# Kernel tuning notes

Measured on AMD Instinct MI355X. Metric: run time of the kernel, lower is better.

## Reference

```python
import jax, jax.numpy as jnp
import numpy as np

KERNEL_DIMS = 16
BOND = 4
OUT = 10
STEP = KERNEL_DIMS // 4          # 4
D = STEP * STEP                  # in_dims = 16
BATCH = 128


def setup_inputs() -> dict:
    key = jax.random.key(0)
    ks = jax.random.split(key, 9)
    d, b = D, BOND
    inp = {
        "inputs": jax.random.normal(ks[0], (BATCH, KERNEL_DIMS, KERNEL_DIMS, 1), dtype=jnp.float32),
        # entanglers (stddev 1e-4 as in the original init)
        "e1": jax.random.normal(ks[1], (d, d, d, d, b, b, b, b), dtype=jnp.float32) * 1e-4,
        "e2": jax.random.normal(ks[2], (b, b, b, b, b, b, b, b), dtype=jnp.float32) * 1e-4,
        # isometries (stddev 1e-5), leg orders exactly as in the source
        "iso1_0": jax.random.normal(ks[3], (d, d, d, b, b), dtype=jnp.float32) * 1e-5,
        "iso1_1": jax.random.normal(ks[4], (d, d, b, d, b), dtype=jnp.float32) * 1e-5,
        "iso1_2": jax.random.normal(ks[5], (d, b, d, d, b), dtype=jnp.float32) * 1e-5,
        "iso1_3": jax.random.normal(ks[6], (b, d, d, d, b), dtype=jnp.float32) * 1e-5,
        "iso2": jax.random.normal(ks[7], (b, b, b, b, OUT), dtype=jnp.float32) * 1e-5,
        "bias": jnp.zeros((OUT,), dtype=jnp.float32),
    }
    return inp


def reference(inputs, e1, e2, iso1_0, iso1_1, iso1_2, iso1_3, iso2, bias):
    B = inputs.shape[0]
    # 4x4 grid of step x step patches, each flattened to D features.
    # patch index k = i*4 + ii, matching the python loops in the original.
    xv = (inputs[..., 0]
          .reshape(B, 4, STEP, 4, STEP)
          .transpose(0, 1, 3, 2, 4)
          .reshape(B, 16, D))           # [B, 16, D]
    p = lambda k: xv[:, k, :]

    # entangler 1: legs 0-3 contract with patches 5,6,9,10; legs 4-7 go to isometries.
    v = jnp.einsum('abcdefgh,Ba,Bb,Bc,Bd->Befgh', e1, p(5), p(6), p(9), p(10))  # [B,b,b,b,b]

    # layer-1 isometries: contract their three patch legs, keep (bond-in m, bond-out o).
    t0 = jnp.einsum('ijkmo,Bi,Bj,Bk->Bmo', iso1_0, p(0), p(1), p(4))    # m = e1 leg4
    t1 = jnp.einsum('ijmko,Bi,Bj,Bk->Bmo', iso1_1, p(2), p(3), p(7))    # m = e1 leg5
    t2 = jnp.einsum('imjko,Bi,Bj,Bk->Bmo', iso1_2, p(8), p(12), p(13))  # m = e1 leg6
    t3 = jnp.einsum('mijko,Bi,Bj,Bk->Bmo', iso1_3, p(11), p(14), p(15)) # m = e1 leg7

    # fuse entangler-1 output with the four isometry bond maps -> entangler-2 inputs.
    w = jnp.einsum('Befgh,Bea,Bfb,Bgc,Bhd->Babcd', v, t0, t1, t2, t3)   # [B,b,b,b,b]

    # entangler 2 then top isometry into output_dims.
    out = jnp.einsum('Babcd,abcdefgh,efghC->BC', w, e2, iso2)           # [B, OUT]
    return out + bias
```

## Files before the change

### kernel.cpp

```cpp
#include <hip/hip_runtime.h>


#define KC 64

typedef __attribute__((ext_vector_type(8))) short bf16x8;
typedef __attribute__((ext_vector_type(4))) float f32x4;

__device__ __forceinline__ void splitf(float x, short& h, short& l) {
    unsigned u = __builtin_bit_cast(unsigned, x);
    h = (short)(u >> 16);
    float hf = __builtin_bit_cast(float, u & 0xFFFF0000u);
    float rem = x - hf;
    l = (short)(__builtin_bit_cast(unsigned, rem) >> 16);
}

__global__ void k1_xv(const float* __restrict__ in, float* __restrict__ xv) {
    int b = blockIdx.x, t = threadIdx.x;
    int k = t >> 4, d = t & 15;
    int row = (k >> 2) * 4 + (d >> 2);
    int col = (k & 3) * 4 + (d & 3);
    xv[b * 256 + t] = in[b * 256 + row * 16 + col];
}

__global__ void __launch_bounds__(256) k2_iso(
        const float* __restrict__ i0, const float* __restrict__ i1,
        const float* __restrict__ i2, const float* __restrict__ i3,
        const float* __restrict__ xv, float* __restrict__ tt) {
    int b = blockIdx.x, iso = blockIdx.y;
    int t = threadIdx.x;

    const int pid0[4] = {0, 2, 8, 11};
    const int pid1[4] = {1, 3, 12, 14};
    const int pid2[4] = {4, 7, 13, 15};
    const int siA[4] = {4096, 4096, 4096, 1024};
    const int sjA[4] = {256, 256, 64, 64};
    const int skA[4] = {16, 4, 4, 4};
    const int smA[4] = {4, 64, 1024, 16384};

    const float* iso_p = (iso == 0) ? i0 : (iso == 1) ? i1 : (iso == 2) ? i2 : i3;

    __shared__ float pX[16], pY[16], pZ[16];
    if (t < 16)      pX[t]      = xv[b * 256 + pid0[iso] * 16 + t];
    else if (t < 32) pY[t - 16] = xv[b * 256 + pid1[iso] * 16 + (t - 16)];
    else if (t < 48) pZ[t - 32] = xv[b * 256 + pid2[iso] * 16 + (t - 32)];
    __syncthreads();

    int i = t >> 4, j = t & 15;
    float pxy = pX[i] * pY[j];
    int sk = skA[iso], sm = smA[iso];
    const float* basep = iso_p + i * siA[iso] + j * sjA[iso];

    float acc[16];
#pragma unroll
    for (int mo = 0; mo < 16; ++mo) acc[mo] = 0.f;

    for (int k = 0; k < 16; ++k) {
        float w = pxy * pZ[k];
        const float* kp = basep + k * sk;
#pragma unroll
        for (int m = 0; m < 4; ++m) {
            float4 v = *(const float4*)(kp + m * sm);
            acc[m * 4 + 0] += w * v.x;
            acc[m * 4 + 1] += w * v.y;
            acc[m * 4 + 2] += w * v.z;
            acc[m * 4 + 3] += w * v.w;
        }
    }

    __shared__ float red[16 * 257];
    __shared__ float part[256];
#pragma unroll
    for (int mo = 0; mo < 16; ++mo) red[mo * 257 + t] = acc[mo];
    __syncthreads();
    int mo = t & 15, seg = t >> 4;
    float s = 0.f;
#pragma unroll
    for (int u = 0; u < 16; ++u) s += red[mo * 257 + seg * 16 + u];
    part[mo * 16 + seg] = s;
    __syncthreads();
    if (t < 16) {
        float o = 0.f;
#pragma unroll
        for (int s2 = 0; s2 < 16; ++s2) o += part[t * 16 + s2];
        tt[iso * 2048 + b * 16 + t] = o;
    }
}

__global__ void k3_m2(const float* __restrict__ e2, const float* __restrict__ iso2,
                      float* __restrict__ M2) {
    __shared__ float is2[2560];
    int t = threadIdx.x;
    for (int s = t; s < 2560; s += 256) is2[s] = iso2[s];
    __syncthreads();
    int flat = blockIdx.x * 256 + t;
    int q = flat / 10, C = flat % 10;
    float acc = 0.f;
    for (int r = 0; r < 256; ++r) acc += e2[q * 256 + r] * is2[r * 10 + C];
    M2[q * 10 + C] = acc;
}

__global__ void __launch_bounds__(256, 1) k4_mfma(const float* __restrict__ e1,
                                                  const float* __restrict__ xv,
                                                  float* __restrict__ vpart) {
    int kc = blockIdx.x;
    int ny = blockIdx.y;
    int tid = threadIdx.x;
    int wv = tid >> 6;
    int lane = tid & 63;
    int mg = wv >> 1;
    int ngr = wv & 1;
    int l15 = lane & 15;
    int g = lane >> 4;
    int d0 = (g & 1) * 8;
    bool hic = (g & 2) != 0;

    float p9r[4][16], p10r[4][8], p5r[4];
#pragma unroll
    for (int t = 0; t < 4; ++t) {
        int b = mg * 64 + t * 16 + l15;
        const float* xb = xv + b * 256;
#pragma unroll
        for (int c = 0; c < 16; ++c) p9r[t][c] = xb[144 + c];
#pragma unroll
        for (int j = 0; j < 8; ++j) p10r[t][j] = xb[160 + d0 + j];
        p5r[t] = xb[80 + (kc >> 2)];
    }

    int colbase = ny * 64 + ngr * 32;
    int col0 = colbase + l15;

    f32x4 acc[4][2];
#pragma unroll
    for (int t = 0; t < 4; ++t)
#pragma unroll
        for (int tn = 0; tn < 2; ++tn)
            acc[t][tn] = (f32x4){0.f, 0.f, 0.f, 0.f};

    const float* ep = e1 + ((size_t)(kc * 1024 + g * 8)) * 256;

    for (int abi = 0; abi < 4; ++abi) {
        int a2 = (kc & 3) * 4 + abi;
        float sab[4];
#pragma unroll
        for (int t = 0; t < 4; ++t) {
            int b = mg * 64 + t * 16 + l15;
            sab[t] = p5r[t] * xv[b * 256 + 96 + a2];
        }
#pragma unroll
        for (int cc = 0; cc < 8; ++cc) {
            bf16x8 eh[2], el[2];
#pragma unroll
            for (int tn = 0; tn < 2; ++tn) {
                const float* ec = ep + (size_t)cc * 32 * 256 + col0 + tn * 16;
#pragma unroll
                for (int j = 0; j < 8; ++j) {
                    float evj = ec[(size_t)j * 256];
                    short h, l; splitf(evj, h, l);
                    eh[tn][j] = h; el[tn][j] = l;
                }
            }
            bf16x8 wh[4], wl[4];
#pragma unroll
            for (int t = 0; t < 4; ++t) {
                float s0 = sab[t] * p9r[t][2 * cc];
                float s1 = sab[t] * p9r[t][2 * cc + 1];
                float s = hic ? s1 : s0;
#pragma unroll
                for (int j = 0; j < 8; ++j) {
                    float wj = s * p10r[t][j];
                    short h, l; splitf(wj, h, l);
                    wh[t][j] = h; wl[t][j] = l;
                }
            }
#pragma unroll
            for (int t = 0; t < 4; ++t)
#pragma unroll
                for (int tn = 0; tn < 2; ++tn) {
                    acc[t][tn] = __builtin_amdgcn_mfma_f32_16x16x32_bf16(wh[t], eh[tn], acc[t][tn], 0, 0, 0);
                    acc[t][tn] = __builtin_amdgcn_mfma_f32_16x16x32_bf16(wh[t], el[tn], acc[t][tn], 0, 0, 0);
                    acc[t][tn] = __builtin_amdgcn_mfma_f32_16x16x32_bf16(wl[t], eh[tn], acc[t][tn], 0, 0, 0);
                }
        }
        ep += (size_t)256 * 256;
    }

#pragma unroll
    for (int t = 0; t < 4; ++t) {
        int brow = mg * 64 + t * 16 + g * 4;
#pragma unroll
        for (int tn = 0; tn < 2; ++tn) {
            int col = colbase + tn * 16 + l15;
#pragma unroll
            for (int r = 0; r < 4; ++r) {
                vpart[((size_t)kc * 128 + brow + r) * 256 + col] = acc[t][tn][r];
            }
        }
    }
}

__global__ void k5_final(const float* __restrict__ vpart, const float* __restrict__ tt,
                         const float* __restrict__ M2, const float* __restrict__ bias,
                         float* __restrict__ out) {
    __shared__ float v[256], A[256], Bb[256];
    __shared__ float t0[16], t1[16], t2[16], t3[16];
    int b = blockIdx.x, t = threadIdx.x;

    float4 s = make_float4(0.f, 0.f, 0.f, 0.f);
    for (int kc = 0; kc < KC; ++kc) {
        float4 pv = *(const float4*)&vpart[((size_t)kc * 128 + b) * 256 + t * 4];
        s.x += pv.x; s.y += pv.y; s.z += pv.z; s.w += pv.w;
    }
    *(float4*)&v[t * 4] = s;
    if (t < 16) {
        t0[t] = tt[0 * 2048 + b * 16 + t];
        t1[t] = tt[1 * 2048 + b * 16 + t];
        t2[t] = tt[2 * 2048 + b * 16 + t];
        t3[t] = tt[3 * 2048 + b * 16 + t];
    }
    __syncthreads();

    for (int q = 0; q < 4; ++q) {
        int idx = t * 4 + q;
        int a = idx >> 6, fgh = idx & 63;
        float acc = 0.f;
        for (int e = 0; e < 4; ++e) acc += t0[e * 4 + a] * v[e * 64 + fgh];
        A[idx] = acc;
    }
    __syncthreads();
    for (int q = 0; q < 4; ++q) {
        int idx = t * 4 + q;
        int a = idx >> 6, bb = (idx >> 4) & 3, gh = idx & 15;
        float acc = 0.f;
        for (int f = 0; f < 4; ++f) acc += t1[f * 4 + bb] * A[a * 64 + f * 16 + gh];
        Bb[idx] = acc;
    }
    __syncthreads();
    for (int q = 0; q < 4; ++q) {
        int idx = t * 4 + q;
        int ab = idx >> 4, c = (idx >> 2) & 3, h = idx & 3;
        float acc = 0.f;
        for (int g = 0; g < 4; ++g) acc += t2[g * 4 + c] * Bb[ab * 16 + g * 4 + h];
        A[idx] = acc;
    }
    __syncthreads();
    for (int q = 0; q < 4; ++q) {
        int idx = t * 4 + q;
        int abc = idx >> 2, dd = idx & 3;
        float acc = 0.f;
        for (int h = 0; h < 4; ++h) acc += t3[h * 4 + dd] * A[abc * 4 + h];
        Bb[idx] = acc;
    }
    __syncthreads();
    if (t < 10) {
        float acc = bias[t];
        for (int q = 0; q < 256; ++q) acc += Bb[q] * M2[q * 10 + t];
        out[b * 10 + t] = acc;
    }
}

extern "C" void kernel_launch(void* const* d_in, const int* in_sizes, int n_in,
                              void* d_out, int out_size, void* d_ws, size_t ws_size,
                              hipStream_t stream) {
    const float* in    = (const float*)d_in[0];
    const float* e1    = (const float*)d_in[1];
    const float* e2    = (const float*)d_in[2];
    const float* iso10 = (const float*)d_in[3];
    const float* iso11 = (const float*)d_in[4];
    const float* iso12 = (const float*)d_in[5];
    const float* iso13 = (const float*)d_in[6];
    const float* iso2  = (const float*)d_in[7];
    const float* bias  = (const float*)d_in[8];
    float* out = (float*)d_out;

    char* ws = (char*)d_ws;
    float* xv    = (float*)(ws + 0);
    float* tt    = (float*)(ws + 131072);
    float* M2    = (float*)(ws + 163840);
    float* vpart = (float*)(ws + 262144);

    hipLaunchKernelGGL(k1_xv, dim3(128), dim3(256), 0, stream, in, xv);
    hipLaunchKernelGGL(k2_iso, dim3(128, 4), dim3(256), 0, stream,
                       iso10, iso11, iso12, iso13, xv, tt);
    hipLaunchKernelGGL(k3_m2, dim3(10), dim3(256), 0, stream, e2, iso2, M2);
    hipLaunchKernelGGL(k4_mfma, dim3(KC, 4), dim3(256), 0, stream, e1, xv, vpart);
    hipLaunchKernelGGL(k5_final, dim3(128), dim3(64), 0, stream,
                       vpart, tt, M2, bias, out);
}
```

Measured before the change: 190.8 us.

## Drop patch-gather kernel and repartition e1 MFMA kernel across more waves

Removes the separate xv gather kernel, so the iso and MFMA kernels index the raw input through a patch-offset helper and one launch disappears. The e1 MFMA kernel now gives each of 8 waves a single 16-row batch tile and 32 columns, launched on a 64x8 grid of 512 threads, in place of 4 waves each holding 4 batch tiles. This cuts per-thread accumulators and registers to raise occupancy and block count. The cost is that each e1 element is now loaded and split to bf16 by every wave instead of being reused across 4 batch tiles, which multiplies that conversion work and the e1 cache traffic. The final kernel moves to 256 threads, one element per thread.

New measurement: 198.7 us. +4.1%, slower.

```diff
diff --git a/kernel.cpp b/kernel.cpp
--- a/kernel.cpp
+++ b/kernel.cpp
@@ -5,6 +5,10 @@
 
 typedef __attribute__((ext_vector_type(8))) short bf16x8;
 typedef __attribute__((ext_vector_type(4))) float f32x4;
+
+__device__ __forceinline__ int poff(int p, int d) {
+    return ((p >> 2) * 4 + (d >> 2)) * 16 + (p & 3) * 4 + (d & 3);
+}
 
 __device__ __forceinline__ void splitf(float x, short& h, short& l) {
     unsigned u = __builtin_bit_cast(unsigned, x);
@@ -14,18 +18,10 @@
     l = (short)(__builtin_bit_cast(unsigned, rem) >> 16);
 }
 
-__global__ void k1_xv(const float* __restrict__ in, float* __restrict__ xv) {
-    int b = blockIdx.x, t = threadIdx.x;
-    int k = t >> 4, d = t & 15;
-    int row = (k >> 2) * 4 + (d >> 2);
-    int col = (k & 3) * 4 + (d & 3);
-    xv[b * 256 + t] = in[b * 256 + row * 16 + col];
-}
-
 __global__ void __launch_bounds__(256) k2_iso(
         const float* __restrict__ i0, const float* __restrict__ i1,
         const float* __restrict__ i2, const float* __restrict__ i3,
-        const float* __restrict__ xv, float* __restrict__ tt) {
+        const float* __restrict__ in, float* __restrict__ tt) {
     int b = blockIdx.x, iso = blockIdx.y;
     int t = threadIdx.x;
 
@@ -40,9 +36,9 @@
     const float* iso_p = (iso == 0) ? i0 : (iso == 1) ? i1 : (iso == 2) ? i2 : i3;
 
     __shared__ float pX[16], pY[16], pZ[16];
-    if (t < 16)      pX[t]      = xv[b * 256 + pid0[iso] * 16 + t];
-    else if (t < 32) pY[t - 16] = xv[b * 256 + pid1[iso] * 16 + (t - 16)];
-    else if (t < 48) pZ[t - 32] = xv[b * 256 + pid2[iso] * 16 + (t - 32)];
+    if (t < 16)      pX[t]      = in[b * 256 + poff(pid0[iso], t)];
+    else if (t < 32) pY[t - 16] = in[b * 256 + poff(pid1[iso], t - 16)];
+    else if (t < 48) pZ[t - 32] = in[b * 256 + poff(pid2[iso], t - 32)];
     __syncthreads();
 
     int i = t >> 4, j = t & 15;
@@ -99,53 +95,47 @@
     M2[q * 10 + C] = acc;
 }
 
-__global__ void __launch_bounds__(256, 1) k4_mfma(const float* __restrict__ e1,
-                                                  const float* __restrict__ xv,
+__global__ void __launch_bounds__(512, 4) k4_mfma(const float* __restrict__ e1,
+                                                  const float* __restrict__ in,
                                                   float* __restrict__ vpart) {
     int kc = blockIdx.x;
     int ny = blockIdx.y;
     int tid = threadIdx.x;
     int wv = tid >> 6;
     int lane = tid & 63;
-    int mg = wv >> 1;
-    int ngr = wv & 1;
     int l15 = lane & 15;
     int g = lane >> 4;
     int d0 = (g & 1) * 8;
     bool hic = (g & 2) != 0;
 
-    float p9r[4][16], p10r[4][8], p5r[4];
-#pragma unroll
-    for (int t = 0; t < 4; ++t) {
-        int b = mg * 64 + t * 16 + l15;
-        const float* xb = xv + b * 256;
-#pragma unroll
-        for (int c = 0; c < 16; ++c) p9r[t][c] = xb[144 + c];
-#pragma unroll
-        for (int j = 0; j < 8; ++j) p10r[t][j] = xb[160 + d0 + j];
-        p5r[t] = xb[80 + (kc >> 2)];
-    }
-
-    int colbase = ny * 64 + ngr * 32;
+    int b = wv * 16 + l15;
+    const float* xb = in + b * 256;
+
+    float p9r[16], p10r[8], p5r;
+#pragma unroll
+    for (int c = 0; c < 16; ++c) p9r[c] = xb[128 + (c >> 2) * 16 + 4 + (c & 3)];
+#pragma unroll
+    for (int j = 0; j < 8; ++j) {
+        int d = d0 + j;
+        p10r[j] = xb[128 + (d >> 2) * 16 + 8 + (d & 3)];
+    }
+    {
+        int a = kc >> 2;
+        p5r = xb[64 + (a >> 2) * 16 + 4 + (a & 3)];
+    }
+
+    int colbase = ny * 32;
     int col0 = colbase + l15;
 
-    f32x4 acc[4][2];
-#pragma unroll
-    for (int t = 0; t < 4; ++t)
-#pragma unroll
-        for (int tn = 0; tn < 2; ++tn)
-            acc[t][tn] = (f32x4){0.f, 0.f, 0.f, 0.f};
+    f32x4 acc[2];
+#pragma unroll
+    for (int tn = 0; tn < 2; ++tn) acc[tn] = (f32x4){0.f, 0.f, 0.f, 0.f};
 
     const float* ep = e1 + ((size_t)(kc * 1024 + g * 8)) * 256;
 
     for (int abi = 0; abi < 4; ++abi) {
         int a2 = (kc & 3) * 4 + abi;
-        float sab[4];
-#pragma unroll
-        for (int t = 0; t < 4; ++t) {
-            int b = mg * 64 + t * 16 + l15;
-            sab[t] = p5r[t] * xv[b * 256 + 96 + a2];
-        }
+        float sab = p5r * xb[64 + (a2 >> 2) * 16 + 8 + (a2 & 3)];
 #pragma unroll
         for (int cc = 0; cc < 8; ++cc) {
             bf16x8 eh[2], el[2];
@@ -159,58 +149,53 @@
                     eh[tn][j] = h; el[tn][j] = l;
                 }
             }
-            bf16x8 wh[4], wl[4];
-#pragma unroll
-            for (int t = 0; t < 4; ++t) {
-                float s0 = sab[t] * p9r[t][2 * cc];
-                float s1 = sab[t] * p9r[t][2 * cc + 1];
+            bf16x8 wh, wl;
+            {
+                float s0 = sab * p9r[2 * cc];
+                float s1 = sab * p9r[2 * cc + 1];
                 float s = hic ? s1 : s0;
 #pragma unroll
                 for (int j = 0; j < 8; ++j) {
-                    float wj = s * p10r[t][j];
+                    float wj = s * p10r[j];
                     short h, l; splitf(wj, h, l);
-                    wh[t][j] = h; wl[t][j] = l;
+                    wh[j] = h; wl[j] = l;
                 }
             }
 #pragma unroll
-            for (int t = 0; t < 4; ++t)
-#pragma unroll
-                for (int tn = 0; tn < 2; ++tn) {
-                    acc[t][tn] = __builtin_amdgcn_mfma_f32_16x16x32_bf16(wh[t], eh[tn], acc[t][tn], 0, 0, 0);
-                    acc[t][tn] = __builtin_amdgcn_mfma_f32_16x16x32_bf16(wh[t], el[tn], acc[t][tn], 0, 0, 0);
-                    acc[t][tn] = __builtin_amdgcn_mfma_f32_16x16x32_bf16(wl[t], eh[tn], acc[t][tn], 0, 0, 0);
-                }
+            for (int tn = 0; tn < 2; ++tn) {
+                acc[tn] = __builtin_amdgcn_mfma_f32_16x16x32_bf16(wh, eh[tn], acc[tn], 0, 0, 0);
+                acc[tn] = __builtin_amdgcn_mfma_f32_16x16x32_bf16(wh, el[tn], acc[tn], 0, 0, 0);
+                acc[tn] = __builtin_amdgcn_mfma_f32_16x16x32_bf16(wl, eh[tn], acc[tn], 0, 0, 0);
+            }
         }
         ep += (size_t)256 * 256;
     }
 
-#pragma unroll
-    for (int t = 0; t < 4; ++t) {
-        int brow = mg * 64 + t * 16 + g * 4;
-#pragma unroll
-        for (int tn = 0; tn < 2; ++tn) {
-            int col = colbase + tn * 16 + l15;
-#pragma unroll
-            for (int r = 0; r < 4; ++r) {
-                vpart[((size_t)kc * 128 + brow + r) * 256 + col] = acc[t][tn][r];
-            }
+    int brow = wv * 16 + g * 4;
+#pragma unroll
+    for (int tn = 0; tn < 2; ++tn) {
+        int col = colbase + tn * 16 + l15;
+#pragma unroll
+        for (int r = 0; r < 4; ++r) {
+            vpart[((size_t)kc * 128 + brow + r) * 256 + col] = acc[tn][r];
         }
     }
 }
 
-__global__ void k5_final(const float* __restrict__ vpart, const float* __restrict__ tt,
-                         const float* __restrict__ M2, const float* __restrict__ bias,
-                         float* __restrict__ out) {
+__global__ void __launch_bounds__(256) k5_final(
+        const float* __restrict__ vpart, const float* __restrict__ tt,
+        const float* __restrict__ M2, const float* __restrict__ bias,
+        float* __restrict__ out) {
     __shared__ float v[256], A[256], Bb[256];
     __shared__ float t0[16], t1[16], t2[16], t3[16];
     int b = blockIdx.x, t = threadIdx.x;
 
-    float4 s = make_float4(0.f, 0.f, 0.f, 0.f);
+    float s = 0.f;
+#pragma unroll 8
     for (int kc = 0; kc < KC; ++kc) {
-        float4 pv = *(const float4*)&vpart[((size_t)kc * 128 + b) * 256 + t * 4];
-        s.x += pv.x; s.y += pv.y; s.z += pv.z; s.w += pv.w;
-    }
-    *(float4*)&v[t * 4] = s;
+        s += vpart[((size_t)kc * 128 + b) * 256 + t];
+    }
+    v[t] = s;
     if (t < 16) {
         t0[t] = tt[0 * 2048 + b * 16 + t];
         t1[t] = tt[1 * 2048 + b * 16 + t];
@@ -219,36 +204,36 @@
     }
     __syncthreads();
 
-    for (int q = 0; q < 4; ++q) {
-        int idx = t * 4 + q;
-        int a = idx >> 6, fgh = idx & 63;
-        float acc = 0.f;
+    {
+        int a = t >> 6, fgh = t & 63;
+        float acc = 0.f;
+#pragma unroll
         for (int e = 0; e < 4; ++e) acc += t0[e * 4 + a] * v[e * 64 + fgh];
-        A[idx] = acc;
-    }
-    __syncthreads();
-    for (int q = 0; q < 4; ++q) {
-        int idx = t * 4 + q;
-        int a = idx >> 6, bb = (idx >> 4) & 3, gh = idx & 15;
-        float acc = 0.f;
+        A[t] = acc;
+    }
+    __syncthreads();
+    {
+        int a = t >> 6, bb = (t >> 4) & 3, gh = t & 15;
+        float acc = 0.f;
+#pragma unroll
         for (int f = 0; f < 4; ++f) acc += t1[f * 4 + bb] * A[a * 64 + f * 16 + gh];
-        Bb[idx] = acc;
-    }
-    __syncthreads();
-    for (int q = 0; q < 4; ++q) {
-        int idx = t * 4 + q;
-        int ab = idx >> 4, c = (idx >> 2) & 3, h = idx & 3;
-        float acc = 0.f;
+        Bb[t] = acc;
+    }
+    __syncthreads();
+    {
+        int ab = t >> 4, c = (t >> 2) & 3, h = t & 3;
+        float acc = 0.f;
+#pragma unroll
         for (int g = 0; g < 4; ++g) acc += t2[g * 4 + c] * Bb[ab * 16 + g * 4 + h];
-        A[idx] = acc;
-    }
-    __syncthreads();
-    for (int q = 0; q < 4; ++q) {
-        int idx = t * 4 + q;
-        int abc = idx >> 2, dd = idx & 3;
-        float acc = 0.f;
+        A[t] = acc;
+    }
+    __syncthreads();
+    {
+        int abc = t >> 2, dd = t & 3;
+        float acc = 0.f;
+#pragma unroll
         for (int h = 0; h < 4; ++h) acc += t3[h * 4 + dd] * A[abc * 4 + h];
-        Bb[idx] = acc;
+        Bb[t] = acc;
     }
     __syncthreads();
     if (t < 10) {
@@ -273,16 +258,14 @@
     float* out = (float*)d_out;
 
     char* ws = (char*)d_ws;
-    float* xv    = (float*)(ws + 0);
     float* tt    = (float*)(ws + 131072);
     float* M2    = (float*)(ws + 163840);
     float* vpart = (float*)(ws + 262144);
 
-    hipLaunchKernelGGL(k1_xv, dim3(128), dim3(256), 0, stream, in, xv);
     hipLaunchKernelGGL(k2_iso, dim3(128, 4), dim3(256), 0, stream,
-                       iso10, iso11, iso12, iso13, xv, tt);
+                       iso10, iso11, iso12, iso13, in, tt);
     hipLaunchKernelGGL(k3_m2, dim3(10), dim3(256), 0, stream, e2, iso2, M2);
-    hipLaunchKernelGGL(k4_mfma, dim3(KC, 4), dim3(256), 0, stream, e1, xv, vpart);
-    hipLaunchKernelGGL(k5_final, dim3(128), dim3(64), 0, stream,
+    hipLaunchKernelGGL(k4_mfma, dim3(KC, 8), dim3(512), 0, stream, e1, in, vpart);
+    hipLaunchKernelGGL(k5_final, dim3(128), dim3(256), 0, stream,
                        vpart, tt, M2, bias, out);
 }
```
